# Performance work log

Hardware: AMD Instinct MI355X
Metric: run time of the kernel (lower is better)

Reference implementation:

```python
import jax, jax.numpy as jnp
import numpy as np


def _conv1d(x, w):
    # x: (B, W, Cin), w: (K, Cin, Cout), SAME padding, stride 1
    return jax.lax.conv_general_dilated(
        x, w, window_strides=(1,), padding='SAME',
        dimension_numbers=('NWC', 'WIO', 'NWC'))


def setup_inputs() -> dict:
    key = jax.random.key(0)
    ks = jax.random.split(key, 5)
    B, T, F, C, K = 64, 64, 256, 64, 9  # batch, num_frames, frame_size(noise_size), filters, kernel
    z = jax.random.normal(ks[0], (B, T, F, 1), dtype=jnp.float32)
    h0 = jax.random.normal(ks[1], (B, F, C), dtype=jnp.float32)
    c0 = jax.random.normal(ks[2], (B, F, C), dtype=jnp.float32)
    Wx = jax.random.normal(ks[3], (K, 1, 4 * C), dtype=jnp.float32) * 0.1
    Wh = jax.random.normal(ks[4], (K, C, 4 * C), dtype=jnp.float32) * 0.1
    b = jnp.zeros((4 * C,), dtype=jnp.float32)
    return {'z': z, 'h0': h0, 'c0': c0, 'Wx': Wx, 'Wh': Wh, 'b': b}


def reference(z, h0, c0, Wx, Wh, b):
    # z: (B, T, F, 1); h0/c0: (B, F, C)
    B = z.shape[0]
    FORGET_BIAS = 1.0  # tf ConvLSTMCell default

    def step(carry, z_t):
        h, c = carry
        gates = _conv1d(z_t, Wx) + _conv1d(h, Wh) + b  # (B, F, 4C)
        i, j, f, o = jnp.split(gates, 4, axis=-1)       # tf gate order: i, new_input, f, o
        c_new = c * jax.nn.sigmoid(f + FORGET_BIAS) + jax.nn.sigmoid(i) * jnp.tanh(j)
        h_new = jnp.tanh(c_new) * jax.nn.sigmoid(o)
        # post_rnn_callback: tanh(mean over channels)
        out = jnp.tanh(jnp.mean(h_new, axis=-1))        # (B, F)
        return (h_new, c_new), out

    z_t_first = jnp.transpose(z, (1, 0, 2, 3))          # (T, B, F, 1)
    (_, _), outs = jax.lax.scan(step, (h0, c0), z_t_first)  # outs: (T, B, F)
    # concat frames along frame axis -> (B, T*F)
    return jnp.transpose(outs, (1, 0, 2)).reshape(B, -1)
```

## Files before the change

### kernel.cpp

```cpp
#include <hip/hip_runtime.h>
#include <hip/hip_bf16.h>

#define BB 64
#define TT 64
#define FF 256
#define CC 64
#define GG 256
#define HP 264
#define GST 264

using frag_ab = __attribute__((ext_vector_type(8))) short;
using f32x4   = __attribute__((ext_vector_type(4))) float;

__device__ __forceinline__ float sigmoidf_(float x) {
    return 1.0f / (1.0f + __expf(-x));
}
__device__ __forceinline__ float tanhf_(float x) {
    const float e = __expf(2.0f * x);
    return 1.0f - 2.0f / (e + 1.0f);
}
__device__ __forceinline__ void split2(float v, short* hi, short* lo) {
    __hip_bfloat16 h = __float2bfloat16(v);
    __hip_bfloat16 l = __float2bfloat16(v - __bfloat162float(h));
    *hi = *reinterpret_cast<short*>(&h);
    *lo = *reinterpret_cast<short*>(&l);
}

__global__ __launch_bounds__(256) void prep_kernel(
    const float* __restrict__ Wh, const float* __restrict__ Wx,
    const float* __restrict__ h0,
    short* __restrict__ WhPh, short* __restrict__ WhPl,
    short* __restrict__ WxTh, short* __restrict__ WxTl,
    short* __restrict__ hAh, short* __restrict__ hAl,
    short* __restrict__ hBh, short* __restrict__ hBl)
{
    const int n = blockIdx.x * 256 + threadIdx.x;
    if (n < BB * HP * CC) {
        const int c = n & 63;
        const int r = (n >> 6) % HP;
        const int b = n / (HP * CC);
        if (r < 4 || r >= 260) {
            hAh[n] = 0; hAl[n] = 0; hBh[n] = 0; hBl[n] = 0;
        } else {
            split2(h0[(b * FF + (r - 4)) * CC + c], &hAh[n], &hAl[n]);
        }
    }
    if (n < 9 * GG * CC) {
        const int c32 = n & 31;
        const int g = (n >> 5) & 255;
        const int p = n >> 13;
        const int k = p >> 1;
        const int cin = (p & 1) * 32 + c32;
        split2(Wh[(k * CC + cin) * GG + g], &WhPh[n], &WhPl[n]);
    }
    if (n < GG * 32) {
        const int kz = n & 31;
        const int g = n >> 5;
        split2(kz < 9 ? Wx[kz * GG + g] : 0.0f, &WxTh[n], &WxTl[n]);
    }
}

__global__ __launch_bounds__(512, 2) void convlstm_step(
    const float* __restrict__ z,
    const short* __restrict__ hinh, const short* __restrict__ hinl,
    const float* __restrict__ c_in,
    const short* __restrict__ WhPh, const short* __restrict__ WhPl,
    const short* __restrict__ WxTh, const short* __restrict__ WxTl,
    const float* __restrict__ bias,
    short* __restrict__ houth, short* __restrict__ houtl,
    float* __restrict__ c_out,
    float* __restrict__ out, int t)
{
    __shared__ __align__(16) char hbyh[72 * 128];
    __shared__ __align__(16) char hbyl[72 * 128];
    __shared__ __align__(16) char zbyh[64 * 64];
    __shared__ __align__(16) char zbyl[64 * 64];
    __shared__ __align__(16) float gbuf[32 * GST];

    const int b = blockIdx.x;
    const int f0 = blockIdx.y * 64;
    const int tid = threadIdx.x;
    const int lane = tid & 63;
    const int w = tid >> 6;

    const int rA = lane & 15;
    const int sA = lane >> 4;
    const int gbase = w * 32;
    const int bln = rA * 32 + sA * 8;

    frag_ab cb[4];
    {
        const int o0 = gbase * 32 + bln;
        cb[0] = *reinterpret_cast<const frag_ab*>(WhPh + o0);
        cb[1] = *reinterpret_cast<const frag_ab*>(WhPh + o0 + 512);
        cb[2] = *reinterpret_cast<const frag_ab*>(WhPl + o0);
        cb[3] = *reinterpret_cast<const frag_ab*>(WhPl + o0 + 512);
    }
    const int flE = tid >> 4;
    const int ch0E = (tid & 15) * 4;
    const int cixE0 = (b * FF + f0 + flE) * CC + ch0E;
    const int cixE1 = cixE0 + 32 * CC;
    const float4 cold0 = *reinterpret_cast<const float4*>(&c_in[cixE0]);
    const float4 cold1 = *reinterpret_cast<const float4*>(&c_in[cixE1]);
    const float bv0 = bias[gbase + rA];
    const float bv1 = bias[gbase + 16 + rA];

    for (int idx = tid; idx < 72 * 8; idx += 512) {
        const int row = idx >> 3, slot = idx & 7;
        const int off = (b * HP + f0 + row) * CC + slot * 8;
        const frag_ab vh = *reinterpret_cast<const frag_ab*>(hinh + off);
        const frag_ab vl = *reinterpret_cast<const frag_ab*>(hinl + off);
        const int a = row * 128 + ((slot ^ (row & 7)) << 4);
        *reinterpret_cast<frag_ab*>(&hbyh[a]) = vh;
        *reinterpret_cast<frag_ab*>(&hbyl[a]) = vl;
    }
    if (tid < 256) {
        const int row = tid >> 2, slot = tid & 3;
        const float* zr = z + ((long)b * TT + t) * FF;
        short vh[8], vl[8];
        #pragma unroll
        for (int j = 0; j < 8; ++j) {
            const int kz = slot * 8 + j;
            const int f = f0 + row - 4 + kz;
            const float val = (kz < 9 && f >= 0 && f < FF) ? zr[f] : 0.0f;
            split2(val, &vh[j], &vl[j]);
        }
        const int a = row * 64 + ((slot ^ (row & 3)) << 4);
        *reinterpret_cast<frag_ab*>(&zbyh[a]) = *reinterpret_cast<frag_ab*>(vh);
        *reinterpret_cast<frag_ab*>(&zbyl[a]) = *reinterpret_cast<frag_ab*>(vl);
    }
    __syncthreads();

    f32x4 acc[4][2];
    #pragma unroll
    for (int Mt = 0; Mt < 4; ++Mt) {
        acc[Mt][0] = (f32x4){bv0, bv0, bv0, bv0};
        acc[Mt][1] = (f32x4){bv1, bv1, bv1, bv1};
    }

    frag_ab cah[4], cal[4];
    #pragma unroll
    for (int Mt = 0; Mt < 4; ++Mt) {
        const int r = Mt * 16 + rA;
        const int a = r * 128 + ((sA ^ (r & 7)) << 4);
        cah[Mt] = *reinterpret_cast<const frag_ab*>(&hbyh[a]);
        cal[Mt] = *reinterpret_cast<const frag_ab*>(&hbyl[a]);
    }

    #pragma unroll
    for (int p = 0; p < 19; ++p) {
        frag_ab nah[4], nal[4], nb[4];
        if (p < 17) {
            const int pn = p + 1;
            const int k = pn >> 1, kk = pn & 1;
            const int sl = kk * 4 + sA;
            #pragma unroll
            for (int Mt = 0; Mt < 4; ++Mt) {
                const int r = Mt * 16 + rA + k;
                const int a = r * 128 + ((sl ^ (r & 7)) << 4);
                nah[Mt] = *reinterpret_cast<const frag_ab*>(&hbyh[a]);
                nal[Mt] = *reinterpret_cast<const frag_ab*>(&hbyl[a]);
            }
            const int o0 = (pn * GG + gbase) * 32 + bln;
            nb[0] = *reinterpret_cast<const frag_ab*>(WhPh + o0);
            nb[1] = *reinterpret_cast<const frag_ab*>(WhPh + o0 + 512);
            nb[2] = *reinterpret_cast<const frag_ab*>(WhPl + o0);
            nb[3] = *reinterpret_cast<const frag_ab*>(WhPl + o0 + 512);
        } else if (p == 17) {
            #pragma unroll
            for (int Mt = 0; Mt < 4; ++Mt) {
                const int r = Mt * 16 + rA;
                const int a = r * 64 + ((sA ^ (r & 3)) << 4);
                nah[Mt] = *reinterpret_cast<const frag_ab*>(&zbyh[a]);
                nal[Mt] = *reinterpret_cast<const frag_ab*>(&zbyl[a]);
            }
            const int o0 = gbase * 32 + bln;
            nb[0] = *reinterpret_cast<const frag_ab*>(WxTh + o0);
            nb[1] = *reinterpret_cast<const frag_ab*>(WxTh + o0 + 512);
            nb[2] = *reinterpret_cast<const frag_ab*>(WxTl + o0);
            nb[3] = *reinterpret_cast<const frag_ab*>(WxTl + o0 + 512);
        }
        __builtin_amdgcn_s_setprio(1);
        #pragma unroll
        for (int Mt = 0; Mt < 4; ++Mt) {
            acc[Mt][0] = __builtin_amdgcn_mfma_f32_16x16x32_bf16(cah[Mt], cb[0], acc[Mt][0], 0, 0, 0);
            acc[Mt][1] = __builtin_amdgcn_mfma_f32_16x16x32_bf16(cah[Mt], cb[1], acc[Mt][1], 0, 0, 0);
        }
        #pragma unroll
        for (int Mt = 0; Mt < 4; ++Mt) {
            acc[Mt][0] = __builtin_amdgcn_mfma_f32_16x16x32_bf16(cah[Mt], cb[2], acc[Mt][0], 0, 0, 0);
            acc[Mt][1] = __builtin_amdgcn_mfma_f32_16x16x32_bf16(cah[Mt], cb[3], acc[Mt][1], 0, 0, 0);
        }
        #pragma unroll
        for (int Mt = 0; Mt < 4; ++Mt) {
            acc[Mt][0] = __builtin_amdgcn_mfma_f32_16x16x32_bf16(cal[Mt], cb[0], acc[Mt][0], 0, 0, 0);
            acc[Mt][1] = __builtin_amdgcn_mfma_f32_16x16x32_bf16(cal[Mt], cb[1], acc[Mt][1], 0, 0, 0);
        }
        __builtin_amdgcn_s_setprio(0);
        if (p < 18) {
            #pragma unroll
            for (int Mt = 0; Mt < 4; ++Mt) { cah[Mt] = nah[Mt]; cal[Mt] = nal[Mt]; }
            cb[0] = nb[0]; cb[1] = nb[1]; cb[2] = nb[2]; cb[3] = nb[3];
        }
    }

    #pragma unroll
    for (int pass = 0; pass < 2; ++pass) {
        if (pass) __syncthreads();
        #pragma unroll
        for (int Mh = 0; Mh < 2; ++Mh) {
            const int Mt = pass * 2 + Mh;
            #pragma unroll
            for (int gtI = 0; gtI < 2; ++gtI) {
                const int g = gbase + gtI * 16 + rA;
                float* gp = &gbuf[(Mh * 16 + sA * 4) * GST + g];
                gp[0]       = acc[Mt][gtI][0];
                gp[GST]     = acc[Mt][gtI][1];
                gp[2 * GST] = acc[Mt][gtI][2];
                gp[3 * GST] = acc[Mt][gtI][3];
            }
        }
        __syncthreads();

        const int f = f0 + pass * 32 + flE;
        const float* gr = &gbuf[flE * GST];
        const f32x4 gi = *reinterpret_cast<const f32x4*>(gr + ch0E);
        const f32x4 gj = *reinterpret_cast<const f32x4*>(gr + 64 + ch0E);
        const f32x4 gf = *reinterpret_cast<const f32x4*>(gr + 128 + ch0E);
        const f32x4 go = *reinterpret_cast<const f32x4*>(gr + 192 + ch0E);

        const float4 cold = pass ? cold1 : cold0;
        const float co_[4] = {cold.x, cold.y, cold.z, cold.w};

        float hsum = 0.0f;
        float cv[4];
        short hh[4], hl[4];
        #pragma unroll
        for (int j = 0; j < 4; ++j) {
            const float cnew = co_[j] * sigmoidf_(gf[j] + 1.0f) + sigmoidf_(gi[j]) * tanhf_(gj[j]);
            const float hnew = tanhf_(cnew) * sigmoidf_(go[j]);
            cv[j] = cnew;
            split2(hnew, &hh[j], &hl[j]);
            hsum += hnew;
        }
        const int cix = (b * FF + f) * CC + ch0E;
        *reinterpret_cast<float4*>(&c_out[cix]) = make_float4(cv[0], cv[1], cv[2], cv[3]);
        const int hix = (b * HP + 4 + f) * CC + ch0E;
        *reinterpret_cast<uint2*>(&houth[hix]) = *reinterpret_cast<uint2*>(hh);
        *reinterpret_cast<uint2*>(&houtl[hix]) = *reinterpret_cast<uint2*>(hl);

        hsum += __shfl_xor(hsum, 1);
        hsum += __shfl_xor(hsum, 2);
        hsum += __shfl_xor(hsum, 4);
        hsum += __shfl_xor(hsum, 8);
        if ((tid & 15) == 0)
            out[(long)b * (TT * FF) + t * FF + f] = tanhf_(hsum * (1.0f / 64.0f));
    }
}

extern "C" void kernel_launch(void* const* d_in, const int* in_sizes, int n_in,
                              void* d_out, int out_size, void* d_ws, size_t ws_size,
                              hipStream_t stream) {
    const float* z    = (const float*)d_in[0];
    const float* h0   = (const float*)d_in[1];
    const float* c0   = (const float*)d_in[2];
    const float* Wx   = (const float*)d_in[3];
    const float* Wh   = (const float*)d_in[4];
    const float* bias = (const float*)d_in[5];
    float* out = (float*)d_out;

    const int SEp = BB * HP * CC;
    const int SE  = BB * FF * CC;
    short* hAh = (short*)d_ws;
    short* hAl = hAh + SEp;
    short* hBh = hAl + SEp;
    short* hBl = hBh + SEp;
    float* cW  = (float*)(hBl + SEp);
    short* WhPh = (short*)(cW + SE);
    short* WhPl = WhPh + 9 * GG * CC;
    short* WxTh = WhPl + 9 * GG * CC;
    short* WxTl = WxTh + GG * 32;

    prep_kernel<<<(SEp + 255) / 256, 256, 0, stream>>>(Wh, Wx, h0, WhPh, WhPl,
                                                       WxTh, WxTl, hAh, hAl, hBh, hBl);

    dim3 grid(BB, FF / 64);
    for (int t = 0; t < TT; ++t) {
        const short* hih = (t & 1) ? hBh : hAh;
        const short* hil = (t & 1) ? hBl : hAl;
        short* hoh = (t & 1) ? hAh : hBh;
        short* hol = (t & 1) ? hAl : hBl;
        const float* cin = (t == 0) ? c0 : cW;
        convlstm_step<<<grid, 512, 0, stream>>>(z, hih, hil, cin,
                                                WhPh, WhPl, WxTh, WxTl, bias,
                                                hoh, hol, cW, out, t);
    }
}
```

Baseline: 1.029 ms.

## Halve frame tile per block to double grid and raise occupancy

```diff
diff --git a/kernel.cpp b/kernel.cpp
--- a/kernel.cpp
+++ b/kernel.cpp
@@ -7,7 +7,8 @@
 #define CC 64
 #define GG 256
 #define HP 264
-#define GST 264
+#define TFR 32
+#define GST 324
 
 using frag_ab = __attribute__((ext_vector_type(8))) short;
 using f32x4   = __attribute__((ext_vector_type(4))) float;
@@ -60,7 +61,7 @@
     }
 }
 
-__global__ __launch_bounds__(512, 2) void convlstm_step(
+__global__ __launch_bounds__(512, 4) void convlstm_step(
     const float* __restrict__ z,
     const short* __restrict__ hinh, const short* __restrict__ hinl,
     const float* __restrict__ c_in,
@@ -71,14 +72,14 @@
     float* __restrict__ c_out,
     float* __restrict__ out, int t)
 {
-    __shared__ __align__(16) char hbyh[72 * 128];
-    __shared__ __align__(16) char hbyl[72 * 128];
-    __shared__ __align__(16) char zbyh[64 * 64];
-    __shared__ __align__(16) char zbyl[64 * 64];
-    __shared__ __align__(16) float gbuf[32 * GST];
+    __shared__ __align__(16) char hbyh[40 * 128];
+    __shared__ __align__(16) char hbyl[40 * 128];
+    __shared__ __align__(16) char zbyh[32 * 64];
+    __shared__ __align__(16) char zbyl[32 * 64];
+    __shared__ __align__(16) float gbuf[TFR * GST];
 
     const int b = blockIdx.x;
-    const int f0 = blockIdx.y * 64;
+    const int f0 = blockIdx.y * TFR;
     const int tid = threadIdx.x;
     const int lane = tid & 63;
     const int w = tid >> 6;
@@ -98,15 +99,13 @@
     }
     const int flE = tid >> 4;
     const int ch0E = (tid & 15) * 4;
-    const int cixE0 = (b * FF + f0 + flE) * CC + ch0E;
-    const int cixE1 = cixE0 + 32 * CC;
-    const float4 cold0 = *reinterpret_cast<const float4*>(&c_in[cixE0]);
-    const float4 cold1 = *reinterpret_cast<const float4*>(&c_in[cixE1]);
+    const int cixE = (b * FF + f0 + flE) * CC + ch0E;
+    const float4 cold = *reinterpret_cast<const float4*>(&c_in[cixE]);
     const float bv0 = bias[gbase + rA];
     const float bv1 = bias[gbase + 16 + rA];
 
-    for (int idx = tid; idx < 72 * 8; idx += 512) {
-        const int row = idx >> 3, slot = idx & 7;
+    if (tid < 40 * 8) {
+        const int row = tid >> 3, slot = tid & 7;
         const int off = (b * HP + f0 + row) * CC + slot * 8;
         const frag_ab vh = *reinterpret_cast<const frag_ab*>(hinh + off);
         const frag_ab vl = *reinterpret_cast<const frag_ab*>(hinl + off);
@@ -114,7 +113,7 @@
         *reinterpret_cast<frag_ab*>(&hbyh[a]) = vh;
         *reinterpret_cast<frag_ab*>(&hbyl[a]) = vl;
     }
-    if (tid < 256) {
+    if (tid < 128) {
         const int row = tid >> 2, slot = tid & 3;
         const float* zr = z + ((long)b * TT + t) * FF;
         short vh[8], vl[8];
@@ -131,131 +130,112 @@
     }
     __syncthreads();
 
-    f32x4 acc[4][2];
-    #pragma unroll
-    for (int Mt = 0; Mt < 4; ++Mt) {
+    f32x4 acc[2][2];
+    #pragma unroll
+    for (int Mt = 0; Mt < 2; ++Mt) {
         acc[Mt][0] = (f32x4){bv0, bv0, bv0, bv0};
         acc[Mt][1] = (f32x4){bv1, bv1, bv1, bv1};
     }
 
-    frag_ab cah[4], cal[4];
-    #pragma unroll
-    for (int Mt = 0; Mt < 4; ++Mt) {
-        const int r = Mt * 16 + rA;
-        const int a = r * 128 + ((sA ^ (r & 7)) << 4);
-        cah[Mt] = *reinterpret_cast<const frag_ab*>(&hbyh[a]);
-        cal[Mt] = *reinterpret_cast<const frag_ab*>(&hbyl[a]);
-    }
-
     #pragma unroll
     for (int p = 0; p < 19; ++p) {
-        frag_ab nah[4], nal[4], nb[4];
+        frag_ab nb[4];
         if (p < 17) {
-            const int pn = p + 1;
-            const int k = pn >> 1, kk = pn & 1;
-            const int sl = kk * 4 + sA;
-            #pragma unroll
-            for (int Mt = 0; Mt < 4; ++Mt) {
-                const int r = Mt * 16 + rA + k;
-                const int a = r * 128 + ((sl ^ (r & 7)) << 4);
-                nah[Mt] = *reinterpret_cast<const frag_ab*>(&hbyh[a]);
-                nal[Mt] = *reinterpret_cast<const frag_ab*>(&hbyl[a]);
-            }
-            const int o0 = (pn * GG + gbase) * 32 + bln;
+            const int o0 = ((p + 1) * GG + gbase) * 32 + bln;
             nb[0] = *reinterpret_cast<const frag_ab*>(WhPh + o0);
             nb[1] = *reinterpret_cast<const frag_ab*>(WhPh + o0 + 512);
             nb[2] = *reinterpret_cast<const frag_ab*>(WhPl + o0);
             nb[3] = *reinterpret_cast<const frag_ab*>(WhPl + o0 + 512);
         } else if (p == 17) {
-            #pragma unroll
-            for (int Mt = 0; Mt < 4; ++Mt) {
-                const int r = Mt * 16 + rA;
-                const int a = r * 64 + ((sA ^ (r & 3)) << 4);
-                nah[Mt] = *reinterpret_cast<const frag_ab*>(&zbyh[a]);
-                nal[Mt] = *reinterpret_cast<const frag_ab*>(&zbyl[a]);
-            }
             const int o0 = gbase * 32 + bln;
             nb[0] = *reinterpret_cast<const frag_ab*>(WxTh + o0);
             nb[1] = *reinterpret_cast<const frag_ab*>(WxTh + o0 + 512);
             nb[2] = *reinterpret_cast<const frag_ab*>(WxTl + o0);
             nb[3] = *reinterpret_cast<const frag_ab*>(WxTl + o0 + 512);
         }
+        frag_ab ah[2], al[2];
+        if (p < 18) {
+            const int k = p >> 1, kk = p & 1;
+            const int sl = kk * 4 + sA;
+            #pragma unroll
+            for (int Mt = 0; Mt < 2; ++Mt) {
+                const int r = Mt * 16 + rA + k;
+                const int a = r * 128 + ((sl ^ (r & 7)) << 4);
+                ah[Mt] = *reinterpret_cast<const frag_ab*>(&hbyh[a]);
+                al[Mt] = *reinterpret_cast<const frag_ab*>(&hbyl[a]);
+            }
+        } else {
+            #pragma unroll
+            for (int Mt = 0; Mt < 2; ++Mt) {
+                const int r = Mt * 16 + rA;
+                const int a = r * 64 + ((sA ^ (r & 3)) << 4);
+                ah[Mt] = *reinterpret_cast<const frag_ab*>(&zbyh[a]);
+                al[Mt] = *reinterpret_cast<const frag_ab*>(&zbyl[a]);
+            }
+        }
         __builtin_amdgcn_s_setprio(1);
         #pragma unroll
-        for (int Mt = 0; Mt < 4; ++Mt) {
-            acc[Mt][0] = __builtin_amdgcn_mfma_f32_16x16x32_bf16(cah[Mt], cb[0], acc[Mt][0], 0, 0, 0);
-            acc[Mt][1] = __builtin_amdgcn_mfma_f32_16x16x32_bf16(cah[Mt], cb[1], acc[Mt][1], 0, 0, 0);
-        }
-        #pragma unroll
-        for (int Mt = 0; Mt < 4; ++Mt) {
-            acc[Mt][0] = __builtin_amdgcn_mfma_f32_16x16x32_bf16(cah[Mt], cb[2], acc[Mt][0], 0, 0, 0);
-            acc[Mt][1] = __builtin_amdgcn_mfma_f32_16x16x32_bf16(cah[Mt], cb[3], acc[Mt][1], 0, 0, 0);
-        }
-        #pragma unroll
-        for (int Mt = 0; Mt < 4; ++Mt) {
-            acc[Mt][0] = __builtin_amdgcn_mfma_f32_16x16x32_bf16(cal[Mt], cb[0], acc[Mt][0], 0, 0, 0);
-            acc[Mt][1] = __builtin_amdgcn_mfma_f32_16x16x32_bf16(cal[Mt], cb[1], acc[Mt][1], 0, 0, 0);
+        for (int Mt = 0; Mt < 2; ++Mt) {
+            acc[Mt][0] = __builtin_amdgcn_mfma_f32_16x16x32_bf16(ah[Mt], cb[0], acc[Mt][0], 0, 0, 0);
+            acc[Mt][1] = __builtin_amdgcn_mfma_f32_16x16x32_bf16(ah[Mt], cb[1], acc[Mt][1], 0, 0, 0);
+        }
+        #pragma unroll
+        for (int Mt = 0; Mt < 2; ++Mt) {
+            acc[Mt][0] = __builtin_amdgcn_mfma_f32_16x16x32_bf16(ah[Mt], cb[2], acc[Mt][0], 0, 0, 0);
+            acc[Mt][1] = __builtin_amdgcn_mfma_f32_16x16x32_bf16(ah[Mt], cb[3], acc[Mt][1], 0, 0, 0);
+        }
+        #pragma unroll
+        for (int Mt = 0; Mt < 2; ++Mt) {
+            acc[Mt][0] = __builtin_amdgcn_mfma_f32_16x16x32_bf16(al[Mt], cb[0], acc[Mt][0], 0, 0, 0);
+            acc[Mt][1] = __builtin_amdgcn_mfma_f32_16x16x32_bf16(al[Mt], cb[1], acc[Mt][1], 0, 0, 0);
         }
         __builtin_amdgcn_s_setprio(0);
-        if (p < 18) {
-            #pragma unroll
-            for (int Mt = 0; Mt < 4; ++Mt) { cah[Mt] = nah[Mt]; cal[Mt] = nal[Mt]; }
-            cb[0] = nb[0]; cb[1] = nb[1]; cb[2] = nb[2]; cb[3] = nb[3];
-        }
-    }
-
-    #pragma unroll
-    for (int pass = 0; pass < 2; ++pass) {
-        if (pass) __syncthreads();
-        #pragma unroll
-        for (int Mh = 0; Mh < 2; ++Mh) {
-            const int Mt = pass * 2 + Mh;
-            #pragma unroll
-            for (int gtI = 0; gtI < 2; ++gtI) {
-                const int g = gbase + gtI * 16 + rA;
-                float* gp = &gbuf[(Mh * 16 + sA * 4) * GST + g];
-                gp[0]       = acc[Mt][gtI][0];
-                gp[GST]     = acc[Mt][gtI][1];
-                gp[2 * GST] = acc[Mt][gtI][2];
-                gp[3 * GST] = acc[Mt][gtI][3];
-            }
-        }
-        __syncthreads();
-
-        const int f = f0 + pass * 32 + flE;
-        const float* gr = &gbuf[flE * GST];
-        const f32x4 gi = *reinterpret_cast<const f32x4*>(gr + ch0E);
-        const f32x4 gj = *reinterpret_cast<const f32x4*>(gr + 64 + ch0E);
-        const f32x4 gf = *reinterpret_cast<const f32x4*>(gr + 128 + ch0E);
-        const f32x4 go = *reinterpret_cast<const f32x4*>(gr + 192 + ch0E);
-
-        const float4 cold = pass ? cold1 : cold0;
-        const float co_[4] = {cold.x, cold.y, cold.z, cold.w};
-
-        float hsum = 0.0f;
-        float cv[4];
-        short hh[4], hl[4];
-        #pragma unroll
-        for (int j = 0; j < 4; ++j) {
-            const float cnew = co_[j] * sigmoidf_(gf[j] + 1.0f) + sigmoidf_(gi[j]) * tanhf_(gj[j]);
-            const float hnew = tanhf_(cnew) * sigmoidf_(go[j]);
-            cv[j] = cnew;
-            split2(hnew, &hh[j], &hl[j]);
-            hsum += hnew;
-        }
-        const int cix = (b * FF + f) * CC + ch0E;
-        *reinterpret_cast<float4*>(&c_out[cix]) = make_float4(cv[0], cv[1], cv[2], cv[3]);
-        const int hix = (b * HP + 4 + f) * CC + ch0E;
-        *reinterpret_cast<uint2*>(&houth[hix]) = *reinterpret_cast<uint2*>(hh);
-        *reinterpret_cast<uint2*>(&houtl[hix]) = *reinterpret_cast<uint2*>(hl);
-
-        hsum += __shfl_xor(hsum, 1);
-        hsum += __shfl_xor(hsum, 2);
-        hsum += __shfl_xor(hsum, 4);
-        hsum += __shfl_xor(hsum, 8);
-        if ((tid & 15) == 0)
-            out[(long)b * (TT * FF) + t * FF + f] = tanhf_(hsum * (1.0f / 64.0f));
-    }
+        if (p < 18) { cb[0] = nb[0]; cb[1] = nb[1]; cb[2] = nb[2]; cb[3] = nb[3]; }
+    }
+
+    #pragma unroll
+    for (int Mt = 0; Mt < 2; ++Mt)
+        #pragma unroll
+        for (int gtI = 0; gtI < 2; ++gtI) {
+            const int g = gbase + gtI * 16 + rA;
+            float* gp = &gbuf[(Mt * 16 + sA * 4) * GST + g];
+            gp[0]       = acc[Mt][gtI][0];
+            gp[GST]     = acc[Mt][gtI][1];
+            gp[2 * GST] = acc[Mt][gtI][2];
+            gp[3 * GST] = acc[Mt][gtI][3];
+        }
+    __syncthreads();
+
+    const int f = f0 + flE;
+    const float* gr = &gbuf[flE * GST];
+    const f32x4 gi = *reinterpret_cast<const f32x4*>(gr + ch0E);
+    const f32x4 gj = *reinterpret_cast<const f32x4*>(gr + 64 + ch0E);
+    const f32x4 gf = *reinterpret_cast<const f32x4*>(gr + 128 + ch0E);
+    const f32x4 go = *reinterpret_cast<const f32x4*>(gr + 192 + ch0E);
+    const float co_[4] = {cold.x, cold.y, cold.z, cold.w};
+
+    float hsum = 0.0f;
+    float cv[4];
+    short hh[4], hl[4];
+    #pragma unroll
+    for (int j = 0; j < 4; ++j) {
+        const float cnew = co_[j] * sigmoidf_(gf[j] + 1.0f) + sigmoidf_(gi[j]) * tanhf_(gj[j]);
+        const float hnew = tanhf_(cnew) * sigmoidf_(go[j]);
+        cv[j] = cnew;
+        split2(hnew, &hh[j], &hl[j]);
+        hsum += hnew;
+    }
+    *reinterpret_cast<float4*>(&c_out[cixE]) = make_float4(cv[0], cv[1], cv[2], cv[3]);
+    const int hix = (b * HP + 4 + f) * CC + ch0E;
+    *reinterpret_cast<uint2*>(&houth[hix]) = *reinterpret_cast<uint2*>(hh);
+    *reinterpret_cast<uint2*>(&houtl[hix]) = *reinterpret_cast<uint2*>(hl);
+
+    hsum += __shfl_xor(hsum, 1);
+    hsum += __shfl_xor(hsum, 2);
+    hsum += __shfl_xor(hsum, 4);
+    hsum += __shfl_xor(hsum, 8);
+    if ((tid & 15) == 0)
+        out[(long)b * (TT * FF) + t * FF + f] = tanhf_(hsum * (1.0f / 64.0f));
 }
 
 extern "C" void kernel_launch(void* const* d_in, const int* in_sizes, int n_in,
@@ -284,7 +264,7 @@
     prep_kernel<<<(SEp + 255) / 256, 256, 0, stream>>>(Wh, Wx, h0, WhPh, WhPl,
                                                        WxTh, WxTl, hAh, hAl, hBh, hBl);
 
-    dim3 grid(BB, FF / 64);
+    dim3 grid(BB, FF / TFR);
     for (int t = 0; t < TT; ++t) {
         const short* hih = (t & 1) ? hBh : hAh;
         const short* hil = (t & 1) ? hBl : hAl;
```

Result: slower. 1.373 ms (+33.5%).

## Halve block to 256 threads with 64 gates per wave and single-pass epilogue

Applied to the files above, without the earlier changes.

```diff
diff --git a/kernel.cpp b/kernel.cpp
--- a/kernel.cpp
+++ b/kernel.cpp
@@ -7,7 +7,7 @@
 #define CC 64
 #define GG 256
 #define HP 264
-#define GST 264
+#define GST 266
 
 using frag_ab = __attribute__((ext_vector_type(8))) short;
 using f32x4   = __attribute__((ext_vector_type(4))) float;
@@ -60,7 +60,7 @@
     }
 }
 
-__global__ __launch_bounds__(512, 2) void convlstm_step(
+__global__ __launch_bounds__(256, 1) void convlstm_step(
     const float* __restrict__ z,
     const short* __restrict__ hinh, const short* __restrict__ hinl,
     const float* __restrict__ c_in,
@@ -75,7 +75,7 @@
     __shared__ __align__(16) char hbyl[72 * 128];
     __shared__ __align__(16) char zbyh[64 * 64];
     __shared__ __align__(16) char zbyl[64 * 64];
-    __shared__ __align__(16) float gbuf[32 * GST];
+    __shared__ __align__(16) float gbuf[64 * GST];
 
     const int b = blockIdx.x;
     const int f0 = blockIdx.y * 64;
@@ -85,27 +85,31 @@
 
     const int rA = lane & 15;
     const int sA = lane >> 4;
-    const int gbase = w * 32;
+    const int gbase = w * 64;
     const int bln = rA * 32 + sA * 8;
 
-    frag_ab cb[4];
+    frag_ab cbh[4], cbl[4];
     {
         const int o0 = gbase * 32 + bln;
-        cb[0] = *reinterpret_cast<const frag_ab*>(WhPh + o0);
-        cb[1] = *reinterpret_cast<const frag_ab*>(WhPh + o0 + 512);
-        cb[2] = *reinterpret_cast<const frag_ab*>(WhPl + o0);
-        cb[3] = *reinterpret_cast<const frag_ab*>(WhPl + o0 + 512);
-    }
-    const int flE = tid >> 4;
-    const int ch0E = (tid & 15) * 4;
-    const int cixE0 = (b * FF + f0 + flE) * CC + ch0E;
-    const int cixE1 = cixE0 + 32 * CC;
-    const float4 cold0 = *reinterpret_cast<const float4*>(&c_in[cixE0]);
-    const float4 cold1 = *reinterpret_cast<const float4*>(&c_in[cixE1]);
-    const float bv0 = bias[gbase + rA];
-    const float bv1 = bias[gbase + 16 + rA];
-
-    for (int idx = tid; idx < 72 * 8; idx += 512) {
+        #pragma unroll
+        for (int gtI = 0; gtI < 4; ++gtI) {
+            cbh[gtI] = *reinterpret_cast<const frag_ab*>(WhPh + o0 + gtI * 512);
+            cbl[gtI] = *reinterpret_cast<const frag_ab*>(WhPl + o0 + gtI * 512);
+        }
+    }
+    float bv[4];
+    #pragma unroll
+    for (int gtI = 0; gtI < 4; ++gtI) bv[gtI] = bias[gbase + gtI * 16 + rA];
+
+    const int flE = tid >> 2;
+    const int chE = (tid & 3) * 16;
+    const int cixE = (b * FF + f0 + flE) * CC + chE;
+    float4 cold[4];
+    #pragma unroll
+    for (int q = 0; q < 4; ++q)
+        cold[q] = *reinterpret_cast<const float4*>(&c_in[cixE + q * 4]);
+
+    for (int idx = tid; idx < 72 * 8; idx += 256) {
         const int row = idx >> 3, slot = idx & 7;
         const int off = (b * HP + f0 + row) * CC + slot * 8;
         const frag_ab vh = *reinterpret_cast<const frag_ab*>(hinh + off);
@@ -114,7 +118,7 @@
         *reinterpret_cast<frag_ab*>(&hbyh[a]) = vh;
         *reinterpret_cast<frag_ab*>(&hbyl[a]) = vl;
     }
-    if (tid < 256) {
+    {
         const int row = tid >> 2, slot = tid & 3;
         const float* zr = z + ((long)b * TT + t) * FF;
         short vh[8], vl[8];
@@ -131,12 +135,12 @@
     }
     __syncthreads();
 
-    f32x4 acc[4][2];
-    #pragma unroll
-    for (int Mt = 0; Mt < 4; ++Mt) {
-        acc[Mt][0] = (f32x4){bv0, bv0, bv0, bv0};
-        acc[Mt][1] = (f32x4){bv1, bv1, bv1, bv1};
-    }
+    f32x4 acc[4][4];
+    #pragma unroll
+    for (int Mt = 0; Mt < 4; ++Mt)
+        #pragma unroll
+        for (int gtI = 0; gtI < 4; ++gtI)
+            acc[Mt][gtI] = (f32x4){bv[gtI], bv[gtI], bv[gtI], bv[gtI]};
 
     frag_ab cah[4], cal[4];
     #pragma unroll
@@ -149,7 +153,7 @@
 
     #pragma unroll
     for (int p = 0; p < 19; ++p) {
-        frag_ab nah[4], nal[4], nb[4];
+        frag_ab nah[4], nal[4], nbh[4], nbl[4];
         if (p < 17) {
             const int pn = p + 1;
             const int k = pn >> 1, kk = pn & 1;
@@ -162,10 +166,11 @@
                 nal[Mt] = *reinterpret_cast<const frag_ab*>(&hbyl[a]);
             }
             const int o0 = (pn * GG + gbase) * 32 + bln;
-            nb[0] = *reinterpret_cast<const frag_ab*>(WhPh + o0);
-            nb[1] = *reinterpret_cast<const frag_ab*>(WhPh + o0 + 512);
-            nb[2] = *reinterpret_cast<const frag_ab*>(WhPl + o0);
-            nb[3] = *reinterpret_cast<const frag_ab*>(WhPl + o0 + 512);
+            #pragma unroll
+            for (int gtI = 0; gtI < 4; ++gtI) {
+                nbh[gtI] = *reinterpret_cast<const frag_ab*>(WhPh + o0 + gtI * 512);
+                nbl[gtI] = *reinterpret_cast<const frag_ab*>(WhPl + o0 + gtI * 512);
+            }
         } else if (p == 17) {
             #pragma unroll
             for (int Mt = 0; Mt < 4; ++Mt) {
@@ -175,85 +180,88 @@
                 nal[Mt] = *reinterpret_cast<const frag_ab*>(&zbyl[a]);
             }
             const int o0 = gbase * 32 + bln;
-            nb[0] = *reinterpret_cast<const frag_ab*>(WxTh + o0);
-            nb[1] = *reinterpret_cast<const frag_ab*>(WxTh + o0 + 512);
-            nb[2] = *reinterpret_cast<const frag_ab*>(WxTl + o0);
-            nb[3] = *reinterpret_cast<const frag_ab*>(WxTl + o0 + 512);
+            #pragma unroll
+            for (int gtI = 0; gtI < 4; ++gtI) {
+                nbh[gtI] = *reinterpret_cast<const frag_ab*>(WxTh + o0 + gtI * 512);
+                nbl[gtI] = *reinterpret_cast<const frag_ab*>(WxTl + o0 + gtI * 512);
+            }
         }
         __builtin_amdgcn_s_setprio(1);
         #pragma unroll
-        for (int Mt = 0; Mt < 4; ++Mt) {
-            acc[Mt][0] = __builtin_amdgcn_mfma_f32_16x16x32_bf16(cah[Mt], cb[0], acc[Mt][0], 0, 0, 0);
-            acc[Mt][1] = __builtin_amdgcn_mfma_f32_16x16x32_bf16(cah[Mt], cb[1], acc[Mt][1], 0, 0, 0);
-        }
-        #pragma unroll
-        for (int Mt = 0; Mt < 4; ++Mt) {
-            acc[Mt][0] = __builtin_amdgcn_mfma_f32_16x16x32_bf16(cah[Mt], cb[2], acc[Mt][0], 0, 0, 0);
-            acc[Mt][1] = __builtin_amdgcn_mfma_f32_16x16x32_bf16(cah[Mt], cb[3], acc[Mt][1], 0, 0, 0);
-        }
-        #pragma unroll
-        for (int Mt = 0; Mt < 4; ++Mt) {
-            acc[Mt][0] = __builtin_amdgcn_mfma_f32_16x16x32_bf16(cal[Mt], cb[0], acc[Mt][0], 0, 0, 0);
-            acc[Mt][1] = __builtin_amdgcn_mfma_f32_16x16x32_bf16(cal[Mt], cb[1], acc[Mt][1], 0, 0, 0);
-        }
+        for (int Mt = 0; Mt < 4; ++Mt)
+            #pragma unroll
+            for (int gtI = 0; gtI < 4; ++gtI)
+                acc[Mt][gtI] = __builtin_amdgcn_mfma_f32_16x16x32_bf16(cah[Mt], cbh[gtI], acc[Mt][gtI], 0, 0, 0);
+        #pragma unroll
+        for (int Mt = 0; Mt < 4; ++Mt)
+            #pragma unroll
+            for (int gtI = 0; gtI < 4; ++gtI)
+                acc[Mt][gtI] = __builtin_amdgcn_mfma_f32_16x16x32_bf16(cah[Mt], cbl[gtI], acc[Mt][gtI], 0, 0, 0);
+        #pragma unroll
+        for (int Mt = 0; Mt < 4; ++Mt)
+            #pragma unroll
+            for (int gtI = 0; gtI < 4; ++gtI)
+                acc[Mt][gtI] = __builtin_amdgcn_mfma_f32_16x16x32_bf16(cal[Mt], cbh[gtI], acc[Mt][gtI], 0, 0, 0);
         __builtin_amdgcn_s_setprio(0);
         if (p < 18) {
             #pragma unroll
-            for (int Mt = 0; Mt < 4; ++Mt) { cah[Mt] = nah[Mt]; cal[Mt] = nal[Mt]; }
-            cb[0] = nb[0]; cb[1] = nb[1]; cb[2] = nb[2]; cb[3] = nb[3];
-        }
-    }
-
-    #pragma unroll
-    for (int pass = 0; pass < 2; ++pass) {
-        if (pass) __syncthreads();
-        #pragma unroll
-        for (int Mh = 0; Mh < 2; ++Mh) {
-            const int Mt = pass * 2 + Mh;
-            #pragma unroll
-            for (int gtI = 0; gtI < 2; ++gtI) {
-                const int g = gbase + gtI * 16 + rA;
-                float* gp = &gbuf[(Mh * 16 + sA * 4) * GST + g];
-                gp[0]       = acc[Mt][gtI][0];
-                gp[GST]     = acc[Mt][gtI][1];
-                gp[2 * GST] = acc[Mt][gtI][2];
-                gp[3 * GST] = acc[Mt][gtI][3];
-            }
-        }
-        __syncthreads();
-
-        const int f = f0 + pass * 32 + flE;
+            for (int q = 0; q < 4; ++q) {
+                cah[q] = nah[q]; cal[q] = nal[q];
+                cbh[q] = nbh[q]; cbl[q] = nbl[q];
+            }
+        }
+    }
+
+    #pragma unroll
+    for (int Mt = 0; Mt < 4; ++Mt)
+        #pragma unroll
+        for (int gtI = 0; gtI < 4; ++gtI) {
+            const int g = gbase + gtI * 16 + rA;
+            float* gp = &gbuf[(Mt * 16 + sA * 4) * GST + g];
+            gp[0]       = acc[Mt][gtI][0];
+            gp[GST]     = acc[Mt][gtI][1];
+            gp[2 * GST] = acc[Mt][gtI][2];
+            gp[3 * GST] = acc[Mt][gtI][3];
+        }
+    __syncthreads();
+
+    {
+        const int f = f0 + flE;
         const float* gr = &gbuf[flE * GST];
-        const f32x4 gi = *reinterpret_cast<const f32x4*>(gr + ch0E);
-        const f32x4 gj = *reinterpret_cast<const f32x4*>(gr + 64 + ch0E);
-        const f32x4 gf = *reinterpret_cast<const f32x4*>(gr + 128 + ch0E);
-        const f32x4 go = *reinterpret_cast<const f32x4*>(gr + 192 + ch0E);
-
-        const float4 cold = pass ? cold1 : cold0;
-        const float co_[4] = {cold.x, cold.y, cold.z, cold.w};
-
+        float cv[16], hv[16];
         float hsum = 0.0f;
-        float cv[4];
-        short hh[4], hl[4];
-        #pragma unroll
-        for (int j = 0; j < 4; ++j) {
-            const float cnew = co_[j] * sigmoidf_(gf[j] + 1.0f) + sigmoidf_(gi[j]) * tanhf_(gj[j]);
-            const float hnew = tanhf_(cnew) * sigmoidf_(go[j]);
-            cv[j] = cnew;
-            split2(hnew, &hh[j], &hl[j]);
-            hsum += hnew;
-        }
-        const int cix = (b * FF + f) * CC + ch0E;
-        *reinterpret_cast<float4*>(&c_out[cix]) = make_float4(cv[0], cv[1], cv[2], cv[3]);
-        const int hix = (b * HP + 4 + f) * CC + ch0E;
-        *reinterpret_cast<uint2*>(&houth[hix]) = *reinterpret_cast<uint2*>(hh);
-        *reinterpret_cast<uint2*>(&houtl[hix]) = *reinterpret_cast<uint2*>(hl);
+        #pragma unroll
+        for (int q = 0; q < 4; ++q) {
+            const f32x4 gi = *reinterpret_cast<const f32x4*>(gr + chE + q * 4);
+            const f32x4 gj = *reinterpret_cast<const f32x4*>(gr + 64 + chE + q * 4);
+            const f32x4 gf = *reinterpret_cast<const f32x4*>(gr + 128 + chE + q * 4);
+            const f32x4 go = *reinterpret_cast<const f32x4*>(gr + 192 + chE + q * 4);
+            const float co_[4] = {cold[q].x, cold[q].y, cold[q].z, cold[q].w};
+            #pragma unroll
+            for (int j = 0; j < 4; ++j) {
+                const float cnew = co_[j] * sigmoidf_(gf[j] + 1.0f) + sigmoidf_(gi[j]) * tanhf_(gj[j]);
+                const float hnew = tanhf_(cnew) * sigmoidf_(go[j]);
+                cv[q * 4 + j] = cnew;
+                hv[q * 4 + j] = hnew;
+                hsum += hnew;
+            }
+        }
+        #pragma unroll
+        for (int q = 0; q < 4; ++q)
+            *reinterpret_cast<float4*>(&c_out[cixE + q * 4]) =
+                make_float4(cv[q*4], cv[q*4+1], cv[q*4+2], cv[q*4+3]);
+        short hh[16], hl[16];
+        #pragma unroll
+        for (int j = 0; j < 16; ++j) split2(hv[j], &hh[j], &hl[j]);
+        const int hix = (b * HP + 4 + f) * CC + chE;
+        *reinterpret_cast<frag_ab*>(&houth[hix])     = *reinterpret_cast<frag_ab*>(hh);
+        *reinterpret_cast<frag_ab*>(&houth[hix + 8]) = *reinterpret_cast<frag_ab*>(hh + 8);
+        *reinterpret_cast<frag_ab*>(&houtl[hix])     = *reinterpret_cast<frag_ab*>(hl);
+        *reinterpret_cast<frag_ab*>(&houtl[hix + 8]) = *reinterpret_cast<frag_ab*>(hl + 8);
 
         hsum += __shfl_xor(hsum, 1);
         hsum += __shfl_xor(hsum, 2);
-        hsum += __shfl_xor(hsum, 4);
-        hsum += __shfl_xor(hsum, 8);
-        if ((tid & 15) == 0)
+        if ((tid & 3) == 0)
             out[(long)b * (TT * FF) + t * FF + f] = tanhf_(hsum * (1.0f / 64.0f));
     }
 }
@@ -291,7 +299,7 @@
         short* hoh = (t & 1) ? hAh : hBh;
         short* hol = (t & 1) ? hAl : hBl;
         const float* cin = (t == 0) ? c0 : cW;
-        convlstm_step<<<grid, 512, 0, stream>>>(z, hih, hil, cin,
+        convlstm_step<<<grid, 256, 0, stream>>>(z, hih, hil, cin,
                                                 WhPh, WhPl, WxTh, WxTl, bias,
                                                 hoh, hol, cW, out, t);
     }
```

Result: slower. 1.110 ms (+7.9%).
